# Performance work log

Measured on AMD Instinct MI355X. Metric: run time of the kernel, lower is better.

The kernel has to match this reference:

```python
import jax, jax.numpy as jnp
import numpy as np

N_NODES = 32768
N_EDGES = 131072
BATCH = 512
SEQ_LEN = 1000
VOCAB = 26  # vocab_size=25 + 1 padding row
EMB = 128


def _bn(x, g, b):
    # BatchNorm1d forward with batch statistics (training-mode math), eps=1e-5
    m = x.mean(0)
    v = x.var(0)
    return g * (x - m) * jax.lax.rsqrt(v + 1e-5) + b


def _gcn(x, src, dst, W, b, n):
    deg = 1.0 + jax.ops.segment_sum(jnp.ones(src.shape[0], x.dtype), dst, num_segments=n)
    dis = jax.lax.rsqrt(deg)
    xw = x @ W
    msg = xw[src] * (dis[src] * dis[dst])[:, None]
    agg = jax.ops.segment_sum(msg, dst, num_segments=n) + xw * (dis * dis)[:, None]
    return agg + b


def _conv1d(x, k, b, pad):
    # x: [B, C_in, L], k: [C_out, C_in, K]
    y = jax.lax.conv_general_dilated(x, k, (1,), [(pad, pad)],
                                     dimension_numbers=('NCH', 'OIH', 'NCH'))
    return y + b[None, :, None]


def setup_inputs() -> dict:
    key = jax.random.key(0)
    ks = jax.random.split(key, 32)
    f = lambda i, shape, s=0.1: (jax.random.normal(ks[i], shape, dtype=jnp.float32) * s)
    inp = {
        'x': jax.random.normal(ks[0], (N_NODES, 5), dtype=jnp.float32),
        'edge_index': jax.random.randint(ks[1], (2, N_EDGES), 0, N_NODES, dtype=jnp.int32),
        'batch': jnp.sort(jax.random.randint(ks[2], (N_NODES,), 0, BATCH, dtype=jnp.int32)),
        'protein_seq': jax.random.randint(ks[3], (BATCH, SEQ_LEN), 0, VOCAB, dtype=jnp.int32),
        # GCN weights
        'W1': f(4, (5, 64)), 'b1': f(5, (64,)),
        'g1': jnp.ones((64,)), 'bt1': jnp.zeros((64,)),
        'W2': f(6, (64, 128)), 'b2': f(7, (128,)),
        'g2': jnp.ones((128,)), 'bt2': jnp.zeros((128,)),
        'W3': f(8, (128, 128)), 'b3': f(9, (128,)),
        'g3': jnp.ones((128,)), 'bt3': jnp.zeros((128,)),
        # protein embedding (row 0 = padding_idx, zeroed)
        'emb': f(10, (VOCAB, EMB)).at[0].set(0.0),
        # protein convs
        'ck1': f(11, (32, 128, 4)), 'cb1': f(12, (32,)),
        'ck2': f(13, (64, 32, 6)), 'cb2': f(14, (64,)),
        'ck3': f(15, (96, 64, 8)), 'cb3': f(16, (96,)),
        'fw1': f(17, (224, 512)), 'fb1': f(18, (512,)),
        'fw2': f(19, (512, 256)), 'fb2': f(20, (256,)),
        'fw3': f(21, (256, 1)), 'fb3': f(22, (1,)),
    }
    return inp


def reference(x, edge_index, batch, protein_seq,
              W1, b1, g1, bt1, W2, b2, g2, bt2, W3, b3, g3, bt3,
              emb, ck1, cb1, ck2, cb2, ck3, cb3,
              fw1, fb1, fw2, fb2, fw3, fb3):
    src, dst = edge_index[0], edge_index[1]
    relu = jax.nn.relu
    # Drug GNN encoder
    h = relu(_bn(_gcn(x, src, dst, W1, b1, N_NODES), g1, bt1))
    h = relu(_bn(_gcn(h, src, dst, W2, b2, N_NODES), g2, bt2))
    h = relu(_bn(_gcn(h, src, dst, W3, b3, N_NODES), g3, bt3))
    cnt = jax.ops.segment_sum(jnp.ones(N_NODES, h.dtype), batch, num_segments=BATCH)
    drug_emb = jax.ops.segment_sum(h, batch, num_segments=BATCH) / jnp.maximum(cnt, 1.0)[:, None]
    # Protein CNN encoder
    e = emb[protein_seq]                    # [B, L, 128]
    p = jnp.transpose(e, (0, 2, 1))         # [B, 128, L]
    p = relu(_conv1d(p, ck1, cb1, 1))       # [B, 32, 999]
    p = relu(_conv1d(p, ck2, cb2, 2))       # [B, 64, 998]
    p = relu(_conv1d(p, ck3, cb3, 3))       # [B, 96, 997]
    prot_emb = p.max(axis=2)                # [B, 96]
    c = jnp.concatenate([drug_emb, prot_emb], axis=1)  # [B, 224]
    c = relu(c @ fw1 + fb1)
    c = relu(c @ fw2 + fb2)
    out = (c @ fw3 + fb3)[:, 0]             # [B]
    return out
```

## Files before the change

### kernel.cpp

```cpp
#include <hip/hip_runtime.h>

#define NN 32768
#define NE 131072
#define NB 512
#define SL 1000

using bf16x8 = __attribute__((ext_vector_type(8))) short;
using f32x4  = __attribute__((ext_vector_type(4))) float;

static __device__ __forceinline__ unsigned short f2b(float f) {
  union { float f; unsigned u; } x; x.f = f;
  unsigned r = x.u + 0x7fffu + ((x.u >> 16) & 1u);
  return (unsigned short)(r >> 16);
}

static __device__ __forceinline__ void bn_from_raw(float sum, float ssq, float g, float b,
                                                   float& sc, float& sh) {
  float m = sum / 32768.f;
  float v = ssq / 32768.f - m * m;
  sc = g * rsqrtf(v + 1e-5f);
  sh = b - m * sc;
}

__global__ void k_degprep(const int* __restrict__ dst, int* __restrict__ degi,
                          const float* __restrict__ emb, const float* __restrict__ ck1,
                          const float* __restrict__ ck2, const float* __restrict__ ck3,
                          unsigned short* __restrict__ emb_bf, unsigned short* __restrict__ wt1,
                          unsigned short* __restrict__ wt2, unsigned short* __restrict__ wt3,
                          float* __restrict__ e1) {
  int gid = blockIdx.x * 256 + threadIdx.x;
  atomicAdd(&degi[dst[gid]], 1);
  int idx = gid;
  if (idx < 3328) {
    emb_bf[idx] = f2b(emb[idx]);
  } else if (idx < 3328 + 16384) {
    int i = idx - 3328;
    int kt = i >> 12, co = (i >> 7) & 31, ci = i & 127;
    wt1[i] = f2b(ck1[co * 512 + ci * 4 + kt]);
  } else if (idx < 3328 + 16384 + 12288) {
    int i = idx - 3328 - 16384;
    int kt = i >> 11, co = (i >> 5) & 63, ci = i & 31;
    wt2[i] = f2b(ck2[co * 192 + ci * 6 + kt]);
  } else if (idx < 3328 + 16384 + 12288 + 49152) {
    int i = idx - 3328 - 16384 - 12288;
    int kt = i / 6144, co = (i >> 6) % 96, ci = i & 63;
    wt3[i] = f2b(ck3[co * 512 + ci * 8 + kt]);
  } else if (idx < 3328 + 16384 + 12288 + 49152 + 3328) {
    int i = idx - 81152;
    int t = i >> 7, kt = (i >> 5) & 3, co = i & 31;
    const float* er = emb + t * 128;
    float s = 0.f;
#pragma unroll 4
    for (int ci = 0; ci < 128; ++ci) s += er[ci] * ck1[co * 512 + ci * 4 + kt];
    e1[i] = s;
  }
}

__global__ void k_scan(const int* __restrict__ degi, int* __restrict__ base,
                       int* __restrict__ cursor, float* __restrict__ dis) {
  __shared__ int part[1024];
  int tid = threadIdx.x;
  int v[32];
  int s = 0;
  int lo = tid * 32;
#pragma unroll
  for (int i = 0; i < 32; ++i) { v[i] = degi[lo + i]; s += v[i]; }
  part[tid] = s;
  __syncthreads();
  for (int off = 1; off < 1024; off <<= 1) {
    int val = (tid >= off) ? part[tid - off] : 0;
    __syncthreads();
    part[tid] += val;
    __syncthreads();
  }
  int run = (tid > 0) ? part[tid - 1] : 0;
#pragma unroll
  for (int i = 0; i < 32; ++i) {
    base[lo + i] = run;
    cursor[lo + i] = run;
    dis[lo + i] = rsqrtf(1.0f + (float)v[i]);
    run += v[i];
  }
  if (tid == 1023) base[NN] = run;
}

__global__ void k_fill(const int* __restrict__ src, const int* __restrict__ dst,
                       int* __restrict__ cursor, unsigned short* __restrict__ csr_src, int E) {
  int e = blockIdx.x * 256 + threadIdx.x;
  if (e < E) {
    int d = dst[e];
    int pos = atomicAdd(&cursor[d], 1);
    csr_src[pos] = (unsigned short)src[e];
  }
}

__launch_bounds__(256)
__global__ void k_gfc1s(const float* __restrict__ x, const float* __restrict__ dis,
                        const int* __restrict__ base, const unsigned short* __restrict__ csr_src,
                        const float* __restrict__ W1, float* __restrict__ out,
                        float* __restrict__ st) {
  __shared__ float sW[5][64];
  __shared__ float a5[256][6];
  __shared__ float red[16][64];
  int tid = threadIdx.x;
  for (int i = tid; i < 320; i += 256) sW[i >> 6][i & 63] = W1[i];
  int n = blockIdx.x * 256 + tid;
  float dn = dis[n];
  float s2 = dn * dn;
  const float* xn = x + (long)n * 5;
  float a0 = xn[0] * s2, a1 = xn[1] * s2, a2 = xn[2] * s2, a3 = xn[3] * s2, a4 = xn[4] * s2;
  int b0 = base[n], b1 = base[n + 1];
  int sNext = (b0 < b1) ? csr_src[b0] : 0;
  for (int j = b0; j < b1; ++j) {
    int s = sNext;
    if (j + 1 < b1) sNext = csr_src[j + 1];
    float coef = dis[s] * dn;
    const float* xs = x + (long)s * 5;
    a0 += xs[0] * coef; a1 += xs[1] * coef; a2 += xs[2] * coef;
    a3 += xs[3] * coef; a4 += xs[4] * coef;
  }
  a5[tid][0] = a0; a5[tid][1] = a1; a5[tid][2] = a2; a5[tid][3] = a3; a5[tid][4] = a4;
  __syncthreads();
  int co = (tid & 15) * 4, strip = tid >> 4;
  float4 s4 = {0.f, 0.f, 0.f, 0.f}, ss4 = {0.f, 0.f, 0.f, 0.f};
  for (int i = 0; i < 16; ++i) {
    int nl = strip * 16 + i;
    long nn = (long)blockIdx.x * 256 + nl;
    float4 acc = {0.f, 0.f, 0.f, 0.f};
#pragma unroll
    for (int ci = 0; ci < 5; ++ci) {
      float av = a5[nl][ci];
      acc.x += av * sW[ci][co];     acc.y += av * sW[ci][co + 1];
      acc.z += av * sW[ci][co + 2]; acc.w += av * sW[ci][co + 3];
    }
    *(float4*)&out[nn * 64 + co] = acc;
    s4.x += acc.x; s4.y += acc.y; s4.z += acc.z; s4.w += acc.w;
    ss4.x += acc.x * acc.x; ss4.y += acc.y * acc.y;
    ss4.z += acc.z * acc.z; ss4.w += acc.w * acc.w;
  }
  *(float4*)&red[strip][co] = s4;
  __syncthreads();
  if (tid < 64) {
    float t = 0.f;
#pragma unroll
    for (int s = 0; s < 16; ++s) t += red[s][tid];
    atomicAdd(&st[tid], t);
  }
  __syncthreads();
  *(float4*)&red[strip][co] = ss4;
  __syncthreads();
  if (tid < 64) {
    float t = 0.f;
#pragma unroll
    for (int s = 0; s < 16; ++s) t += red[s][tid];
    atomicAdd(&st[64 + tid], t);
  }
}

template<int C>
__launch_bounds__(256)
__global__ void k_gbngather(const float* __restrict__ in, const float* __restrict__ dis,
                            const int* __restrict__ base, const unsigned short* __restrict__ csr_src,
                            const float* __restrict__ st, const float* __restrict__ g,
                            const float* __restrict__ bt, float* __restrict__ out) {
  constexpr int TPN = C / 4;
  int t = blockIdx.x * 256 + threadIdx.x;
  int n = t / TPN;
  int c = (t % TPN) * 4;
  float4 sum4 = *(const float4*)&st[c];
  float4 ssq4 = *(const float4*)&st[C + c];
  float4 gg = *(const float4*)&g[c];
  float4 bb = *(const float4*)&bt[c];
  float4 sc4, sh4;
  bn_from_raw(sum4.x, ssq4.x, gg.x, bb.x, sc4.x, sh4.x);
  bn_from_raw(sum4.y, ssq4.y, gg.y, bb.y, sc4.y, sh4.y);
  bn_from_raw(sum4.z, ssq4.z, gg.z, bb.z, sc4.z, sh4.z);
  bn_from_raw(sum4.w, ssq4.w, gg.w, bb.w, sc4.w, sh4.w);
  float dn = dis[n];
  float s2 = dn * dn;
  float4 a = *(const float4*)&in[(long)n * C + c];
  float4 acc;
  acc.x = fmaxf(a.x * sc4.x + sh4.x, 0.f) * s2;
  acc.y = fmaxf(a.y * sc4.y + sh4.y, 0.f) * s2;
  acc.z = fmaxf(a.z * sc4.z + sh4.z, 0.f) * s2;
  acc.w = fmaxf(a.w * sc4.w + sh4.w, 0.f) * s2;
  int b0 = base[n], b1 = base[n + 1];
  int sNext = (b0 < b1) ? csr_src[b0] : 0;
  for (int j = b0; j < b1; ++j) {
    int s = sNext;
    if (j + 1 < b1) sNext = csr_src[j + 1];
    float coef = dis[s] * dn;
    float4 vv = *(const float4*)&in[(long)s * C + c];
    acc.x += fmaxf(vv.x * sc4.x + sh4.x, 0.f) * coef;
    acc.y += fmaxf(vv.y * sc4.y + sh4.y, 0.f) * coef;
    acc.z += fmaxf(vv.z * sc4.z + sh4.z, 0.f) * coef;
    acc.w += fmaxf(vv.w * sc4.w + sh4.w, 0.f) * coef;
  }
  *(float4*)&out[(long)n * C + c] = acc;
}

template<int C_OUT, int K, int TN, bool RELU, bool BIAS, bool STATS>
__launch_bounds__(256)
__global__ void k_fc4(const float* __restrict__ in, const float* __restrict__ W,
                      const float* __restrict__ bias, float* __restrict__ out,
                      float* __restrict__ st, int N) {
  constexpr int CO4 = C_OUT / 4;
  constexpr int GPB = 256 / CO4;
  int g = blockIdx.x * GPB + threadIdx.x / CO4;
  long n0 = (long)g * TN;
  if (!STATS && n0 >= N) return;
  int co = (threadIdx.x % CO4) * 4;
  float4 acc[TN];
  float4 b4 = {0.f, 0.f, 0.f, 0.f};
  if (BIAS) b4 = *(const float4*)&bias[co];
#pragma unroll
  for (int t = 0; t < TN; ++t) acc[t] = b4;
  for (int ci = 0; ci < K; ci += 4) {
    float4 w0 = *(const float4*)&W[(long)(ci + 0) * C_OUT + co];
    float4 w1 = *(const float4*)&W[(long)(ci + 1) * C_OUT + co];
    float4 w2 = *(const float4*)&W[(long)(ci + 2) * C_OUT + co];
    float4 w3 = *(const float4*)&W[(long)(ci + 3) * C_OUT + co];
#pragma unroll
    for (int t = 0; t < TN; ++t) {
      float4 a = *(const float4*)&in[(n0 + t) * K + ci];
      acc[t].x += a.x * w0.x; acc[t].y += a.x * w0.y; acc[t].z += a.x * w0.z; acc[t].w += a.x * w0.w;
      acc[t].x += a.y * w1.x; acc[t].y += a.y * w1.y; acc[t].z += a.y * w1.z; acc[t].w += a.y * w1.w;
      acc[t].x += a.z * w2.x; acc[t].y += a.z * w2.y; acc[t].z += a.z * w2.z; acc[t].w += a.z * w2.w;
      acc[t].x += a.w * w3.x; acc[t].y += a.w * w3.y; acc[t].z += a.w * w3.z; acc[t].w += a.w * w3.w;
    }
  }
  float4 s4 = {0.f, 0.f, 0.f, 0.f}, ss4 = {0.f, 0.f, 0.f, 0.f};
#pragma unroll
  for (int t = 0; t < TN; ++t) {
    float4 o = acc[t];
    if (RELU) {
      o.x = fmaxf(o.x, 0.f); o.y = fmaxf(o.y, 0.f);
      o.z = fmaxf(o.z, 0.f); o.w = fmaxf(o.w, 0.f);
    }
    *(float4*)&out[(n0 + t) * C_OUT + co] = o;
    if (STATS) {
      s4.x += o.x; s4.y += o.y; s4.z += o.z; s4.w += o.w;
      ss4.x += o.x * o.x; ss4.y += o.y * o.y;
      ss4.z += o.z * o.z; ss4.w += o.w * o.w;
    }
  }
  if (STATS) {
    __shared__ float red2[GPB][C_OUT];
    int grp = threadIdx.x / CO4;
    *(float4*)&red2[grp][co] = s4;
    __syncthreads();
    if (threadIdx.x < C_OUT) {
      float t = 0.f;
#pragma unroll
      for (int s = 0; s < GPB; ++s) t += red2[s][threadIdx.x];
      atomicAdd(&st[threadIdx.x], t);
    }
    __syncthreads();
    *(float4*)&red2[grp][co] = ss4;
    __syncthreads();
    if (threadIdx.x < C_OUT) {
      float t = 0.f;
#pragma unroll
      for (int s = 0; s < GPB; ++s) t += red2[s][threadIdx.x];
      atomicAdd(&st[C_OUT + threadIdx.x], t);
    }
  }
}

__launch_bounds__(256)
__global__ void k_reg(const float* __restrict__ cbuf,
                      const float* __restrict__ fw1, const float* __restrict__ fb1,
                      const float* __restrict__ fw2, const float* __restrict__ fb2,
                      const float* __restrict__ fw3, const float* __restrict__ fb3,
                      float* __restrict__ out) {
  __shared__ float cin[224];
  __shared__ float h1[512];
  __shared__ float h2[256];
  __shared__ float red[4];
  int b = blockIdx.x, t = threadIdx.x;
  if (t < 224) cin[t] = cbuf[b * 224 + t];
  __syncthreads();
  {
    float a0 = fb1[t], a1 = fb1[t + 256];
    for (int ci = 0; ci < 224; ++ci) {
      float av = cin[ci];
      a0 += av * fw1[ci * 512 + t];
      a1 += av * fw1[ci * 512 + t + 256];
    }
    h1[t] = fmaxf(a0, 0.f);
    h1[t + 256] = fmaxf(a1, 0.f);
  }
  __syncthreads();
  {
    float a = fb2[t];
    for (int ci = 0; ci < 512; ++ci) a += h1[ci] * fw2[ci * 256 + t];
    h2[t] = fmaxf(a, 0.f);
  }
  __syncthreads();
  {
    float p = h2[t] * fw3[t];
#pragma unroll
    for (int off = 32; off > 0; off >>= 1) p += __shfl_down(p, off, 64);
    if ((t & 63) == 0) red[t >> 6] = p;
    __syncthreads();
    if (t == 0) out[b] = red[0] + red[1] + red[2] + red[3] + fb3[0];
  }
}

__launch_bounds__(256, 3)
__global__ void conv_mfma(const int* __restrict__ seq, const float* __restrict__ e1g,
                          const float* __restrict__ cb1,
                          const unsigned short* __restrict__ wt2g, const float* __restrict__ cb2,
                          const unsigned short* __restrict__ wt3g, const float* __restrict__ cb3,
                          const float* __restrict__ agg, const float* __restrict__ st3,
                          const float* __restrict__ g3, const float* __restrict__ bt3,
                          const int* __restrict__ batch, float* __restrict__ outmax) {
  __shared__ __align__(16) unsigned short s_w[12288];
  __shared__ __align__(16) unsigned short s_c1[4864];
  __shared__ __align__(16) unsigned short s_c2[9216];
  __shared__ int s_tok[152];
  __shared__ int s_max[96];

  int tid = threadIdx.x;
  int b = blockIdx.y;

  if (blockIdx.x == 8) {
    __shared__ int s_lo, s_hi;
    if (tid == 0) {
      int lo = 0, hi = NN;
      while (lo < hi) { int m = (lo + hi) >> 1; if (batch[m] < b) lo = m + 1; else hi = m; }
      s_lo = lo;
      hi = NN;
      while (lo < hi) { int m = (lo + hi) >> 1; if (batch[m] <= b) lo = m + 1; else hi = m; }
      s_hi = lo;
    }
    __syncthreads();
    if (tid < 128) {
      int lo = s_lo, hi = s_hi, c = tid;
      float sc, sh;
      bn_from_raw(st3[c], st3[128 + c], g3[c], bt3[c], sc, sh);
      float s = 0.f;
      for (int n = lo; n < hi; ++n) s += fmaxf(agg[(long)n * 128 + c] * sc + sh, 0.f);
      outmax[b * 224 + c] = s / fmaxf((float)(hi - lo), 1.0f);
    }
    return;
  }

  int t0 = blockIdx.x * 128;

  if (tid < 96) s_max[tid] = 0;
  if (tid < 152) {
    int p = t0 - 6 + tid;
    s_tok[tid] = (p >= 0 && p < SL) ? seq[b * SL + p] : 0;
  }
  if (tid < 128) ((int*)(s_c1 + 144 * 32))[tid] = 0;

  {
#pragma unroll
    for (int c = 0; c < 6; ++c) {
      int ch = c * 256 + tid;
      int row = ch >> 2;
      *(bf16x8*)&s_w[row * 32 + (((row ^ ch) & 3) << 3)] = *(const bf16x8*)(wt2g + ch * 8);
    }
  }
  __syncthreads();

  int lane = tid & 63, wave = tid >> 6;
  int l15 = lane & 15, quad = lane >> 4;

  {
    bool edge = (blockIdx.x == 0) || (blockIdx.x == 7);
#pragma unroll
    for (int pass = 0; pass < 2; ++pass) {
      int m = (pass == 0) ? (tid >> 1) : (128 + (tid >> 1));
      bool act = (pass == 0) || (tid < 32);
      if (act) {
        int co0 = (tid & 1) * 16;
        f32x4 a4[4];
#pragma unroll
        for (int q = 0; q < 4; ++q) a4[q] = *(const f32x4*)&cb1[co0 + q * 4];
#pragma unroll
        for (int kt = 0; kt < 4; ++kt) {
          const float* e = e1g + s_tok[m + kt] * 128 + kt * 32 + co0;
#pragma unroll
          for (int q = 0; q < 4; ++q) {
            f32x4 v = *(const f32x4*)&e[q * 4];
            a4[q][0] += v[0]; a4[q][1] += v[1]; a4[q][2] += v[2]; a4[q][3] += v[3];
          }
        }
        int l1 = t0 - 5 + m;
        bool ok = !edge || (l1 >= 0 && l1 < 999);
#pragma unroll
        for (int q = 0; q < 4; ++q) {
#pragma unroll
          for (int e2 = 0; e2 < 4; e2 += 2) {
            int co = co0 + q * 4 + e2;
            unsigned lo = ok ? (unsigned)f2b(fmaxf(a4[q][e2], 0.f)) : 0u;
            unsigned hi = ok ? (unsigned)f2b(fmaxf(a4[q][e2 + 1], 0.f)) : 0u;
            *(unsigned*)&s_c1[m * 32 + ((((co >> 3) ^ m) & 3) << 3) + (co & 7)] = lo | (hi << 16);
          }
        }
      }
    }
  }
  __syncthreads();

  {
    int mt0 = wave, mt1 = wave + 4;
    f32x4 acc[2][4];
#pragma unroll
    for (int nt = 0; nt < 4; ++nt) {
      float bv = cb2[nt * 16 + l15];
      acc[0][nt] = (f32x4){bv, bv, bv, bv};
      acc[1][nt] = (f32x4){bv, bv, bv, bv};
    }
    for (int kt = 0; kt < 6; ++kt) {
      int r0 = mt0 * 16 + l15 + kt, r1 = mt1 * 16 + l15 + kt;
      bf16x8 a0 = *(const bf16x8*)&s_c1[r0 * 32 + (((quad ^ r0) & 3) << 3)];
      bf16x8 a1 = *(const bf16x8*)&s_c1[r1 * 32 + (((quad ^ r1) & 3) << 3)];
#pragma unroll
      for (int nt = 0; nt < 4; ++nt) {
        int wr = kt * 64 + nt * 16 + l15;
        bf16x8 bf = *(const bf16x8*)&s_w[wr * 32 + (((quad ^ wr) & 3) << 3)];
        acc[0][nt] = __builtin_amdgcn_mfma_f32_16x16x32_bf16(a0, bf, acc[0][nt], 0, 0, 0);
        acc[1][nt] = __builtin_amdgcn_mfma_f32_16x16x32_bf16(a1, bf, acc[1][nt], 0, 0, 0);
      }
    }
#pragma unroll
    for (int mb = 0; mb < 2; ++mb) {
      int mt = mb ? mt1 : mt0;
#pragma unroll
      for (int nt = 0; nt < 4; ++nt) {
        int co = nt * 16 + l15;
#pragma unroll
        for (int r = 0; r < 4; ++r) {
          int m = mt * 16 + quad * 4 + r;
          int l2 = t0 - 3 + m;
          unsigned short hv = f2b(fmaxf(acc[mb][nt][r], 0.f));
          s_c2[m * 64 + ((((co >> 3) ^ m) & 7) << 3) + (co & 7)] = (l2 >= 0 && l2 < 998) ? hv : (unsigned short)0;
        }
      }
    }
    if (wave == 0) {
      f32x4 acc8[4];
#pragma unroll
      for (int nt = 0; nt < 4; ++nt) {
        float bv = cb2[nt * 16 + l15];
        acc8[nt] = (f32x4){bv, bv, bv, bv};
      }
      for (int kt = 0; kt < 6; ++kt) {
        int r0 = 128 + l15 + kt;
        bf16x8 a0 = *(const bf16x8*)&s_c1[r0 * 32 + (((quad ^ r0) & 3) << 3)];
#pragma unroll
        for (int nt = 0; nt < 4; ++nt) {
          int wr = kt * 64 + nt * 16 + l15;
          bf16x8 bf = *(const bf16x8*)&s_w[wr * 32 + (((quad ^ wr) & 3) << 3)];
          acc8[nt] = __builtin_amdgcn_mfma_f32_16x16x32_bf16(a0, bf, acc8[nt], 0, 0, 0);
        }
      }
#pragma unroll
      for (int nt = 0; nt < 4; ++nt) {
        int co = nt * 16 + l15;
#pragma unroll
        for (int r = 0; r < 4; ++r) {
          int m = 128 + quad * 4 + r;
          int l2 = t0 - 3 + m;
          unsigned short hv = f2b(fmaxf(acc8[nt][r], 0.f));
          s_c2[m * 64 + ((((co >> 3) ^ m) & 7) << 3) + (co & 7)] = (l2 >= 0 && l2 < 998) ? hv : (unsigned short)0;
        }
      }
    }
  }

  {
    bf16x8 w3t[3];
#pragma unroll
    for (int c = 0; c < 3; ++c) w3t[c] = *(const bf16x8*)(wt3g + (c * 256 + tid) * 8);
    __syncthreads();
#pragma unroll
    for (int c = 0; c < 3; ++c) {
      int ch = c * 256 + tid;
      int row = ch >> 3;
      *(bf16x8*)&s_w[row * 64 + (((row ^ ch) & 7) << 3)] = w3t[c];
    }
    __syncthreads();
  }

  {
    int mt0 = wave, mt1 = wave + 4;
    f32x4 acc[2][6];
#pragma unroll
    for (int nt = 0; nt < 6; ++nt) {
      float bv = cb3[nt * 16 + l15];
      acc[0][nt] = (f32x4){bv, bv, bv, bv};
      acc[1][nt] = (f32x4){bv, bv, bv, bv};
    }
    for (int kt = 0; kt < 8; ++kt) {
      bf16x8 w3t[3];
      if (kt < 7) {
#pragma unroll
        for (int c = 0; c < 3; ++c)
          w3t[c] = *(const bf16x8*)(wt3g + ((kt + 1) * 768 + c * 256 + tid) * 8);
      }
      int bo = (kt & 1) * 6144;
      int ra0 = mt0 * 16 + l15 + kt, ra1 = mt1 * 16 + l15 + kt;
#pragma unroll
      for (int cb = 0; cb < 2; ++cb) {
        bf16x8 a0 = *(const bf16x8*)&s_c2[ra0 * 64 + ((((cb * 4 + quad) ^ ra0) & 7) << 3)];
        bf16x8 a1 = *(const bf16x8*)&s_c2[ra1 * 64 + ((((cb * 4 + quad) ^ ra1) & 7) << 3)];
#pragma unroll
        for (int nt = 0; nt < 6; ++nt) {
          int wr = nt * 16 + l15;
          bf16x8 bf = *(const bf16x8*)&s_w[bo + wr * 64 + ((((cb * 4 + quad) ^ wr) & 7) << 3)];
          acc[0][nt] = __builtin_amdgcn_mfma_f32_16x16x32_bf16(a0, bf, acc[0][nt], 0, 0, 0);
          acc[1][nt] = __builtin_amdgcn_mfma_f32_16x16x32_bf16(a1, bf, acc[1][nt], 0, 0, 0);
        }
      }
      if (kt < 7) {
        int bo2 = 6144 - bo;
#pragma unroll
        for (int c = 0; c < 3; ++c) {
          int ch = c * 256 + tid;
          int row = ch >> 3;
          *(bf16x8*)&s_w[bo2 + row * 64 + (((row ^ ch) & 7) << 3)] = w3t[c];
        }
      }
      __syncthreads();
    }
#pragma unroll
    for (int nt = 0; nt < 6; ++nt) {
      int co = nt * 16 + l15;
      float mx = 0.f;
#pragma unroll
      for (int mb = 0; mb < 2; ++mb) {
        int mt = mb ? mt1 : mt0;
#pragma unroll
        for (int r = 0; r < 4; ++r) {
          int l3 = t0 + mt * 16 + quad * 4 + r;
          if (l3 < 997) mx = fmaxf(mx, acc[mb][nt][r]);
        }
      }
      atomicMax(&s_max[co], __float_as_int(mx));
    }
  }
  __syncthreads();
  if (tid < 96) atomicMax((int*)&outmax[b * 224 + 128 + tid], s_max[tid]);
}

extern "C" void kernel_launch(void* const* d_in, const int* in_sizes, int n_in,
                              void* d_out, int out_size, void* d_ws, size_t ws_size,
                              hipStream_t stream) {
  (void)in_sizes; (void)n_in; (void)out_size; (void)ws_size;
  const float* x = (const float*)d_in[0];
  const int* ei = (const int*)d_in[1];
  const int* batch = (const int*)d_in[2];
  const int* seq = (const int*)d_in[3];
  const float* W1 = (const float*)d_in[4];
  const float* g1 = (const float*)d_in[6];
  const float* bt1 = (const float*)d_in[7];
  const float* W2 = (const float*)d_in[8];
  const float* g2 = (const float*)d_in[10];
  const float* bt2 = (const float*)d_in[11];
  const float* W3 = (const float*)d_in[12];
  const float* g3 = (const float*)d_in[14];
  const float* bt3 = (const float*)d_in[15];
  const float* emb = (const float*)d_in[16];
  const float* ck1 = (const float*)d_in[17];
  const float* cb1 = (const float*)d_in[18];
  const float* ck2 = (const float*)d_in[19];
  const float* cb2 = (const float*)d_in[20];
  const float* ck3 = (const float*)d_in[21];
  const float* cb3 = (const float*)d_in[22];
  const float* fw1 = (const float*)d_in[23];
  const float* fb1 = (const float*)d_in[24];
  const float* fw2 = (const float*)d_in[25];
  const float* fb2 = (const float*)d_in[26];
  const float* fw3 = (const float*)d_in[27];
  const float* fb3 = (const float*)d_in[28];
  const int* src = ei;
  const int* dst = ei + NE;

  float* ws = (float*)d_ws;
  float* bufA = ws;
  float* bufB = ws + 4194304;
  float* dis = ws + 8388608;
  float* stats = ws + 8421376;
  float* cbuf = ws + 8422032;
  int* degi = (int*)(ws + 8536720);
  int* base = degi + NN;
  int* cursor = base + NN + 1;
  unsigned short* csr_src = (unsigned short*)(cursor + NN);
  unsigned short* emb_bf = (unsigned short*)(ws + 8700564);
  unsigned short* wt1 = emb_bf + 3328;
  unsigned short* wt2 = wt1 + 16384;
  unsigned short* wt3 = wt2 + 12288;
  float* e1 = ws + 8741140;
  float* out = (float*)d_out;

  hipMemsetAsync(stats, 0, (656 + 114688 + 32768) * sizeof(float), stream);

  k_degprep<<<NE / 256, 256, 0, stream>>>(dst, degi, emb, ck1, ck2, ck3, emb_bf, wt1, wt2, wt3, e1);
  k_scan<<<1, 1024, 0, stream>>>(degi, base, cursor, dis);
  k_fill<<<NE / 256, 256, 0, stream>>>(src, dst, cursor, csr_src, NE);

  k_gfc1s<<<NN / 256, 256, 0, stream>>>(x, dis, base, csr_src, W1, bufA, stats);
  k_gbngather<64><<<NN * 16 / 256, 256, 0, stream>>>(bufA, dis, base, csr_src, stats, g1, bt1, bufB);
  k_fc4<128, 64, 4, false, false, true><<<1024, 256, 0, stream>>>(bufB, W2, nullptr, bufA, stats + 128, NN);
  k_gbngather<128><<<NN * 32 / 256, 256, 0, stream>>>(bufA, dis, base, csr_src, stats + 128, g2, bt2, bufB);
  k_fc4<128, 128, 4, false, false, true><<<1024, 256, 0, stream>>>(bufB, W3, nullptr, bufA, stats + 384, NN);

  conv_mfma<<<dim3(9, NB), 256, 0, stream>>>(seq, e1, cb1, wt2, cb2, wt3, cb3,
                                             bufA, stats + 384, g3, bt3, batch, cbuf);

  k_reg<<<NB, 256, 0, stream>>>(cbuf, fw1, fb1, fw2, fb2, fw3, fb3, out);
}
```

Baseline: 408.3 us.

## Split first GCN layer into per-channel gather and FC, batch regressor rows, drop dead prep

The first GCN layer's fused gather+FC kernel is split in two. A gather kernel now uses one thread per (node, input channel), which raises parallelism and coalescing. A separate FC kernel maps 16 nodes per block and accumulates BN statistics with more atomics. The regressor now handles two batch rows per block so each weight load is reused twice, halving weight traffic. Unused bf16 conversions of the embedding and conv1 weights are removed from the prep kernel. The cost is one extra launch and an intermediate buffer round trip.

```diff
diff --git a/kernel.cpp b/kernel.cpp
--- a/kernel.cpp
+++ b/kernel.cpp
@@ -25,28 +25,21 @@
 __global__ void k_degprep(const int* __restrict__ dst, int* __restrict__ degi,
                           const float* __restrict__ emb, const float* __restrict__ ck1,
                           const float* __restrict__ ck2, const float* __restrict__ ck3,
-                          unsigned short* __restrict__ emb_bf, unsigned short* __restrict__ wt1,
                           unsigned short* __restrict__ wt2, unsigned short* __restrict__ wt3,
                           float* __restrict__ e1) {
   int gid = blockIdx.x * 256 + threadIdx.x;
   atomicAdd(&degi[dst[gid]], 1);
   int idx = gid;
-  if (idx < 3328) {
-    emb_bf[idx] = f2b(emb[idx]);
-  } else if (idx < 3328 + 16384) {
-    int i = idx - 3328;
-    int kt = i >> 12, co = (i >> 7) & 31, ci = i & 127;
-    wt1[i] = f2b(ck1[co * 512 + ci * 4 + kt]);
-  } else if (idx < 3328 + 16384 + 12288) {
-    int i = idx - 3328 - 16384;
+  if (idx < 12288) {
+    int i = idx;
     int kt = i >> 11, co = (i >> 5) & 63, ci = i & 31;
     wt2[i] = f2b(ck2[co * 192 + ci * 6 + kt]);
-  } else if (idx < 3328 + 16384 + 12288 + 49152) {
-    int i = idx - 3328 - 16384 - 12288;
+  } else if (idx < 12288 + 49152) {
+    int i = idx - 12288;
     int kt = i / 6144, co = (i >> 6) % 96, ci = i & 63;
     wt3[i] = f2b(ck3[co * 512 + ci * 8 + kt]);
-  } else if (idx < 3328 + 16384 + 12288 + 49152 + 3328) {
-    int i = idx - 81152;
+  } else if (idx < 12288 + 49152 + 3328) {
+    int i = idx - 61440;
     int t = i >> 7, kt = (i >> 5) & 3, co = i & 31;
     const float* er = emb + t * 128;
     float s = 0.f;
@@ -95,50 +88,46 @@
 }
 
 __launch_bounds__(256)
-__global__ void k_gfc1s(const float* __restrict__ x, const float* __restrict__ dis,
+__global__ void k_gagg5(const float* __restrict__ x, const float* __restrict__ dis,
                         const int* __restrict__ base, const unsigned short* __restrict__ csr_src,
-                        const float* __restrict__ W1, float* __restrict__ out,
-                        float* __restrict__ st) {
-  __shared__ float sW[5][64];
-  __shared__ float a5[256][6];
-  __shared__ float red[16][64];
-  int tid = threadIdx.x;
-  for (int i = tid; i < 320; i += 256) sW[i >> 6][i & 63] = W1[i];
-  int n = blockIdx.x * 256 + tid;
+                        float* __restrict__ a5g) {
+  int t = blockIdx.x * 256 + threadIdx.x;
+  int n = t / 5, c = t - n * 5;
   float dn = dis[n];
-  float s2 = dn * dn;
-  const float* xn = x + (long)n * 5;
-  float a0 = xn[0] * s2, a1 = xn[1] * s2, a2 = xn[2] * s2, a3 = xn[3] * s2, a4 = xn[4] * s2;
+  float a = x[t] * (dn * dn);
   int b0 = base[n], b1 = base[n + 1];
   int sNext = (b0 < b1) ? csr_src[b0] : 0;
   for (int j = b0; j < b1; ++j) {
     int s = sNext;
     if (j + 1 < b1) sNext = csr_src[j + 1];
-    float coef = dis[s] * dn;
-    const float* xs = x + (long)s * 5;
-    a0 += xs[0] * coef; a1 += xs[1] * coef; a2 += xs[2] * coef;
-    a3 += xs[3] * coef; a4 += xs[4] * coef;
-  }
-  a5[tid][0] = a0; a5[tid][1] = a1; a5[tid][2] = a2; a5[tid][3] = a3; a5[tid][4] = a4;
-  __syncthreads();
-  int co = (tid & 15) * 4, strip = tid >> 4;
-  float4 s4 = {0.f, 0.f, 0.f, 0.f}, ss4 = {0.f, 0.f, 0.f, 0.f};
-  for (int i = 0; i < 16; ++i) {
-    int nl = strip * 16 + i;
-    long nn = (long)blockIdx.x * 256 + nl;
-    float4 acc = {0.f, 0.f, 0.f, 0.f};
-#pragma unroll
-    for (int ci = 0; ci < 5; ++ci) {
-      float av = a5[nl][ci];
-      acc.x += av * sW[ci][co];     acc.y += av * sW[ci][co + 1];
-      acc.z += av * sW[ci][co + 2]; acc.w += av * sW[ci][co + 3];
-    }
-    *(float4*)&out[nn * 64 + co] = acc;
-    s4.x += acc.x; s4.y += acc.y; s4.z += acc.z; s4.w += acc.w;
-    ss4.x += acc.x * acc.x; ss4.y += acc.y * acc.y;
-    ss4.z += acc.z * acc.z; ss4.w += acc.w * acc.w;
-  }
-  *(float4*)&red[strip][co] = s4;
+    a += x[s * 5 + c] * (dis[s] * dn);
+  }
+  a5g[t] = a;
+}
+
+__launch_bounds__(256)
+__global__ void k_fc5s(const float* __restrict__ a5g, const float* __restrict__ W1,
+                       float* __restrict__ out, float* __restrict__ st) {
+  __shared__ float sW[5][64];
+  __shared__ float red[16][64];
+  int tid = threadIdx.x;
+  for (int i = tid; i < 320; i += 256) sW[i >> 6][i & 63] = W1[i];
+  __syncthreads();
+  int grp = tid >> 4;
+  int co = (tid & 15) * 4;
+  long n = (long)blockIdx.x * 16 + grp;
+  float a[5];
+#pragma unroll
+  for (int ci = 0; ci < 5; ++ci) a[ci] = a5g[n * 5 + ci];
+  float4 acc = {0.f, 0.f, 0.f, 0.f};
+#pragma unroll
+  for (int ci = 0; ci < 5; ++ci) {
+    float av = a[ci];
+    acc.x += av * sW[ci][co];     acc.y += av * sW[ci][co + 1];
+    acc.z += av * sW[ci][co + 2]; acc.w += av * sW[ci][co + 3];
+  }
+  *(float4*)&out[n * 64 + co] = acc;
+  *(float4*)&red[grp][co] = acc;
   __syncthreads();
   if (tid < 64) {
     float t = 0.f;
@@ -147,7 +136,9 @@
     atomicAdd(&st[tid], t);
   }
   __syncthreads();
-  *(float4*)&red[strip][co] = ss4;
+  float4 ss;
+  ss.x = acc.x * acc.x; ss.y = acc.y * acc.y; ss.z = acc.z * acc.z; ss.w = acc.w * acc.w;
+  *(float4*)&red[grp][co] = ss;
   __syncthreads();
   if (tid < 64) {
     float t = 0.f;
@@ -273,37 +264,53 @@
                       const float* __restrict__ fw2, const float* __restrict__ fb2,
                       const float* __restrict__ fw3, const float* __restrict__ fb3,
                       float* __restrict__ out) {
-  __shared__ float cin[224];
-  __shared__ float h1[512];
-  __shared__ float h2[256];
-  __shared__ float red[4];
-  int b = blockIdx.x, t = threadIdx.x;
-  if (t < 224) cin[t] = cbuf[b * 224 + t];
-  __syncthreads();
-  {
-    float a0 = fb1[t], a1 = fb1[t + 256];
+  __shared__ float cin[2][224];
+  __shared__ float h1[2][512];
+  __shared__ float h2[2][256];
+  __shared__ float red[2][4];
+  int b = blockIdx.x * 2, t = threadIdx.x;
+  if (t < 224) {
+    cin[0][t] = cbuf[b * 224 + t];
+    cin[1][t] = cbuf[(b + 1) * 224 + t];
+  }
+  __syncthreads();
+  {
+    float b0v = fb1[t], b1v = fb1[t + 256];
+    float a00 = b0v, a01 = b1v, a10 = b0v, a11 = b1v;
     for (int ci = 0; ci < 224; ++ci) {
-      float av = cin[ci];
-      a0 += av * fw1[ci * 512 + t];
-      a1 += av * fw1[ci * 512 + t + 256];
-    }
-    h1[t] = fmaxf(a0, 0.f);
-    h1[t + 256] = fmaxf(a1, 0.f);
-  }
-  __syncthreads();
-  {
-    float a = fb2[t];
-    for (int ci = 0; ci < 512; ++ci) a += h1[ci] * fw2[ci * 256 + t];
-    h2[t] = fmaxf(a, 0.f);
-  }
-  __syncthreads();
-  {
-    float p = h2[t] * fw3[t];
-#pragma unroll
-    for (int off = 32; off > 0; off >>= 1) p += __shfl_down(p, off, 64);
-    if ((t & 63) == 0) red[t >> 6] = p;
-    __syncthreads();
-    if (t == 0) out[b] = red[0] + red[1] + red[2] + red[3] + fb3[0];
+      float w0 = fw1[ci * 512 + t];
+      float w1 = fw1[ci * 512 + t + 256];
+      float av0 = cin[0][ci], av1 = cin[1][ci];
+      a00 += av0 * w0; a01 += av0 * w1;
+      a10 += av1 * w0; a11 += av1 * w1;
+    }
+    h1[0][t] = fmaxf(a00, 0.f); h1[0][t + 256] = fmaxf(a01, 0.f);
+    h1[1][t] = fmaxf(a10, 0.f); h1[1][t + 256] = fmaxf(a11, 0.f);
+  }
+  __syncthreads();
+  {
+    float a0 = fb2[t], a1 = fb2[t];
+    for (int ci = 0; ci < 512; ++ci) {
+      float w = fw2[ci * 256 + t];
+      a0 += h1[0][ci] * w;
+      a1 += h1[1][ci] * w;
+    }
+    h2[0][t] = fmaxf(a0, 0.f);
+    h2[1][t] = fmaxf(a1, 0.f);
+  }
+  __syncthreads();
+  {
+    float w3 = fw3[t];
+    float p0 = h2[0][t] * w3, p1 = h2[1][t] * w3;
+#pragma unroll
+    for (int off = 32; off > 0; off >>= 1) {
+      p0 += __shfl_down(p0, off, 64);
+      p1 += __shfl_down(p1, off, 64);
+    }
+    if ((t & 63) == 0) { red[0][t >> 6] = p0; red[1][t >> 6] = p1; }
+    __syncthreads();
+    if (t == 0) out[b] = red[0][0] + red[0][1] + red[0][2] + red[0][3] + fb3[0];
+    if (t == 1) out[b + 1] = red[1][0] + red[1][1] + red[1][2] + red[1][3] + fb3[0];
   }
 }
 
@@ -595,15 +602,17 @@
   unsigned short* wt2 = wt1 + 16384;
   unsigned short* wt3 = wt2 + 12288;
   float* e1 = ws + 8741140;
+  float* a5g = bufB;
   float* out = (float*)d_out;
 
   hipMemsetAsync(stats, 0, (656 + 114688 + 32768) * sizeof(float), stream);
 
-  k_degprep<<<NE / 256, 256, 0, stream>>>(dst, degi, emb, ck1, ck2, ck3, emb_bf, wt1, wt2, wt3, e1);
+  k_degprep<<<NE / 256, 256, 0, stream>>>(dst, degi, emb, ck1, ck2, ck3, wt2, wt3, e1);
   k_scan<<<1, 1024, 0, stream>>>(degi, base, cursor, dis);
   k_fill<<<NE / 256, 256, 0, stream>>>(src, dst, cursor, csr_src, NE);
 
-  k_gfc1s<<<NN / 256, 256, 0, stream>>>(x, dis, base, csr_src, W1, bufA, stats);
+  k_gagg5<<<NN * 5 / 256, 256, 0, stream>>>(x, dis, base, csr_src, a5g);
+  k_fc5s<<<NN / 16, 256, 0, stream>>>(a5g, W1, bufA, stats);
   k_gbngather<64><<<NN * 16 / 256, 256, 0, stream>>>(bufA, dis, base, csr_src, stats, g1, bt1, bufB);
   k_fc4<128, 64, 4, false, false, true><<<1024, 256, 0, stream>>>(bufB, W2, nullptr, bufA, stats + 128, NN);
   k_gbngather<128><<<NN * 32 / 256, 256, 0, stream>>>(bufA, dis, base, csr_src, stats + 128, g2, bt2, bufB);
@@ -612,5 +621,5 @@
   conv_mfma<<<dim3(9, NB), 256, 0, stream>>>(seq, e1, cb1, wt2, cb2, wt3, cb3,
                                              bufA, stats + 384, g3, bt3, batch, cbuf);
 
-  k_reg<<<NB, 256, 0, stream>>>(cbuf, fw1, fb1, fw2, fb2, fw3, fb3, out);
-}
+  k_reg<<<NB / 2, 256, 0, stream>>>(cbuf, fw1, fb1, fw2, fb2, fw3, fb3, out);
+}
```

After: 469.9 us. 1.15x slower.
